# Kernel optimization log

Measured on AMD Instinct MI355X. Metric: run time of the kernel, lower is better.

## Reference

```python
import jax, jax.numpy as jnp
import numpy as np

B_, C_, H_, W_, Dd_ = 2, 64, 32, 32, 32
D_INNER, D_STATE, DT_RANK, D_CONV = 64, 8, 4, 4


def setup_inputs() -> dict:
    key = jax.random.key(0)
    ks = jax.random.split(key, 12)
    s = 0.05
    A_init = jnp.log(jnp.tile(jnp.arange(1, D_STATE + 1, dtype=jnp.float32), (D_INNER, 1)))
    return {
        "input": jax.random.normal(ks[0], (B_, C_, H_, W_, Dd_), jnp.float32),
        "conv_w": jax.random.normal(ks[1], (C_, C_, 3, 3, 3), jnp.float32) * s,
        "conv_b": jax.random.normal(ks[2], (C_,), jnp.float32) * s,
        "in_proj_w": jax.random.normal(ks[3], (2 * D_INNER, C_), jnp.float32) * s,
        "conv1d_w": jax.random.normal(ks[4], (D_INNER, 1, D_CONV), jnp.float32) * s,
        "conv1d_b": jax.random.normal(ks[5], (D_INNER,), jnp.float32) * s,
        "x_proj_w": jax.random.normal(ks[6], (DT_RANK + 2 * D_STATE, D_INNER), jnp.float32) * s,
        "dt_proj_w": jax.random.normal(ks[7], (D_INNER, DT_RANK), jnp.float32) * s,
        "dt_proj_b": jax.random.normal(ks[8], (D_INNER,), jnp.float32) * s,
        "A_log": A_init,
        "A_b_log": A_init + 0.01,
        "D_skip": jnp.ones((D_INNER,), jnp.float32),
        "out_proj_w": jax.random.normal(ks[9], (C_, D_INNER), jnp.float32) * s,
        "ln_g": jnp.ones((C_,), jnp.float32),
        "ln_b": jnp.zeros((C_,), jnp.float32),
    }


def _conv3d(x, w, b):
    y = jax.lax.conv_general_dilated(x, w, (1, 1, 1), [(1, 1), (1, 1), (1, 1)],
                                     dimension_numbers=("NCDHW", "OIDHW", "NCDHW"))
    return y + b[None, :, None, None, None]


def _instance_norm(x, eps=1e-5):
    m = x.mean(axis=(2, 3, 4), keepdims=True)
    v = ((x - m) ** 2).mean(axis=(2, 3, 4), keepdims=True)
    return (x - m) * jax.lax.rsqrt(v + eps)


def _selective_scan(xc, dt, Bm, Cm, A, D_skip):
    # xc, dt: (b,L,d); Bm, Cm: (b,L,n); A: (d,n)
    dA = jnp.exp(dt[..., None] * A)                       # (b,L,d,n)
    dBx = (dt * xc)[..., None] * Bm[:, :, None, :]        # (b,L,d,n)

    def comb(l, r):
        al, bl = l
        ar, br = r
        return ar * al, ar * bl + br

    _, h = jax.lax.associative_scan(comb, (dA, dBx), axis=1)
    y = jnp.einsum("bldn,bln->bld", h, Cm)
    return y + xc * D_skip


def _direction(xz, conv1d_w, conv1d_b, x_proj_w, dt_proj_w, dt_proj_b, A, D_skip):
    x, z = jnp.split(xz, 2, axis=-1)                      # each (b,L,d)
    xt = jnp.swapaxes(x, 1, 2)                            # (b,d,L)
    xc = jax.lax.conv_general_dilated(xt, conv1d_w, (1,), [(D_CONV - 1, 0)],
                                      feature_group_count=D_INNER,
                                      dimension_numbers=("NCH", "OIH", "NCH"))
    xc = jax.nn.silu(jnp.swapaxes(xc + conv1d_b[None, :, None], 1, 2))  # (b,L,d)
    dbl = xc @ x_proj_w.T
    dt_r = dbl[..., :DT_RANK]
    Bm = dbl[..., DT_RANK:DT_RANK + D_STATE]
    Cm = dbl[..., DT_RANK + D_STATE:]
    dt = jax.nn.softplus(dt_r @ dt_proj_w.T + dt_proj_b)
    y = _selective_scan(xc, dt, Bm, Cm, A, D_skip)
    return y * jax.nn.silu(z)


def reference(input, conv_w, conv_b, in_proj_w, conv1d_w, conv1d_b, x_proj_w,
              dt_proj_w, dt_proj_b, A_log, A_b_log, D_skip, out_proj_w, ln_g, ln_b):
    # skip path: Conv3d -> InstanceNorm3d -> ReLU
    skip = jax.nn.relu(_instance_norm(_conv3d(input, conv_w, conv_b)))
    b, c, h, w, d = input.shape
    tokens = input.transpose(0, 2, 3, 4, 1).reshape(b, h * w * d, c)  # b (hwd) c
    xz = tokens @ in_proj_w.T                                          # (b,L,2d)
    A = -jnp.exp(A_log)
    A_b = -jnp.exp(A_b_log)
    y_f = _direction(xz, conv1d_w, conv1d_b, x_proj_w, dt_proj_w, dt_proj_b, A, D_skip)
    y_b = _direction(xz[:, ::-1], conv1d_w, conv1d_b, x_proj_w, dt_proj_w, dt_proj_b, A_b, D_skip)[:, ::-1]
    out = ((y_f + y_b) @ out_proj_w.T) / 2.0  # if_devide_out=True
    mu = out.mean(-1, keepdims=True)
    var = ((out - mu) ** 2).mean(-1, keepdims=True)
    out = (out - mu) * jax.lax.rsqrt(var + 1e-5) * ln_g + ln_b  # use_norm=True
    vol = out.reshape(b, h, w, d, c).transpose(0, 4, 1, 2, 3)
    return _conv3d(vol, conv_w, conv_b) + skip
```

## Files before the change

kernel.cpp:

```cpp
#include <hip/hip_runtime.h>
#include <hip/hip_bf16.h>

typedef __hip_bfloat16 bf16;
typedef __attribute__((ext_vector_type(8))) short short8;
typedef __attribute__((ext_vector_type(4))) float f32x4;

__device__ __forceinline__ float b2f(bf16 x){ return __bfloat162float(x); }
__device__ __forceinline__ bf16  f2b(float x){ return __float2bfloat16(x); }
__device__ __forceinline__ float s2f(short s){ bf16 t = *(bf16*)&s; return b2f(t); }

__device__ __forceinline__ float ldin(const void* p, size_t i, int f32){
  return f32 ? ((const float*)p)[i] : b2f(((const bf16*)p)[i]);
}
__device__ __forceinline__ void stout(void* p, size_t i, float v, int f32){
  if(f32) ((float*)p)[i] = v; else ((bf16*)p)[i] = f2b(v);
}

constexpr int SP   = 32*32*32;
constexpr int LTOK = SP;
constexpr int NC   = 512;
constexpr int CLEN = LTOK / NC;
constexpr int NSEQ = 2*2*64*8;
constexpr int SEG  = 16;
constexpr int SEGLEN = NC/SEG;

__global__ void k_detect(const void* conv_w, int* flag){
  if(threadIdx.x==0 && blockIdx.x==0){
    const bf16* p = (const bf16*)conv_w;
    int f = 0;
    for(int i=0;i<128;i++){
      float v = b2f(p[i]);
      if(!(v==v) || fabsf(v) > 1.0f) f = 1;
    }
    *flag = f;
  }
}

__global__ void k_fill(void* out, int n, const int* flag){
  const int f32 = *flag;
  int i = blockIdx.x*256 + threadIdx.x;
  if(i<n) stout(out, i, 12345.0f, f32);
}

__global__ void k_wprep(const void* __restrict__ cw, bf16* __restrict__ wt,
                        const int* __restrict__ flag){
  const int f32 = *flag;
  int t = blockIdx.x*256 + threadIdx.x;
  if(t >= 27*64*64) return;
  int tap = t >> 12;
  int oc  = (t >> 6) & 63;
  int ci  = t & 63;
  wt[t] = f2b(ldin(cw, ((size_t)(oc*64+ci))*27 + tap, f32));
}

__global__ __launch_bounds__(256) void k_inprojm(
    const void* __restrict__ in, const void* __restrict__ pw,
    bf16* __restrict__ xz, bf16* __restrict__ xin_t,
    const int* __restrict__ flag){
  const int f32 = *flag;
  __shared__ bf16 tok[128*72];
  __shared__ bf16 wl [128*72];
  int tid = threadIdx.x;
  int b = blockIdx.x >> 8, tile = blockIdx.x & 255;
  int l0 = tile*128;

  for(int p=tid; p<1024; p+=256){
    int j = p & 127, c8 = p >> 7;
    short8 v;
    #pragma unroll
    for(int k=0;k<8;k++){
      bf16 t = f2b(ldin(pw, j*64 + c8*8 + k, f32));
      v[k] = *(short*)&t;
    }
    *(short8*)(&wl[j*72 + c8*8]) = v;
  }
  for(int p=tid; p<1024; p+=256){
    int i = p & 127, c8 = p >> 7;
    short8 v;
    #pragma unroll
    for(int k=0;k<8;k++){
      bf16 t = f2b(ldin(in, ((size_t)(b*64 + c8*8 + k))*SP + l0 + i, f32));
      v[k] = *(short*)&t;
    }
    *(short8*)(&tok[i*72 + c8*8]) = v;
  }
  __syncthreads();

  int lane = tid & 63, wv = tid >> 6;
  int pn = lane & 15, quad = lane >> 4, kg8 = quad*8;
  f32x4 acc[2][8];
  #pragma unroll
  for(int mt=0;mt<2;mt++)
    #pragma unroll
    for(int nt=0;nt<8;nt++) acc[mt][nt]=(f32x4)(0.f);

  #pragma unroll
  for(int kq=0;kq<2;kq++){
    short8 a0 = *(const short8*)(&tok[(wv*32      + pn)*72 + kq*32 + kg8]);
    short8 a1 = *(const short8*)(&tok[(wv*32 + 16 + pn)*72 + kq*32 + kg8]);
    #pragma unroll
    for(int nt=0;nt<8;nt++){
      short8 bb = *(const short8*)(&wl[(nt*16+pn)*72 + kq*32 + kg8]);
      acc[0][nt] = __builtin_amdgcn_mfma_f32_16x16x32_bf16(a0,bb,acc[0][nt],0,0,0);
      acc[1][nt] = __builtin_amdgcn_mfma_f32_16x16x32_bf16(a1,bb,acc[1][nt],0,0,0);
    }
  }

  #pragma unroll
  for(int mt=0;mt<2;mt++){
    #pragma unroll
    for(int nt=0;nt<8;nt++){
      #pragma unroll
      for(int r=0;r<4;r++){
        int token = wv*32 + mt*16 + quad*4 + r;
        xz[((size_t)b*LTOK + l0 + token)*128 + nt*16 + pn] = f2b(acc[mt][nt][r]);
      }
    }
  }
  for(int p=tid; p<8192; p+=256){
    int i = p >> 6, c = p & 63;
    xin_t[((size_t)b*SP + l0 + i)*64 + c] = tok[i*72 + c];
  }
}

__global__ __launch_bounds__(256, 2) void k_convm(
    const bf16* __restrict__ xin_t, const bf16* __restrict__ wt,
    const void* __restrict__ cb, const bf16* __restrict__ skip,
    bf16* __restrict__ out_bf, void* __restrict__ out_any,
    int mode, const int* __restrict__ flag){
  const int f32 = *flag;
  __shared__ bf16 xt[612*40];

  int tid  = threadIdx.x;
  int lane = tid & 63;
  int wv   = tid >> 6;
  int pn   = lane & 15;
  int quad = lane >> 4;
  int kg8  = quad * 8;
  int laneA = pn*64 + kg8;

  int blk = blockIdx.x;
  int b  = blk >> 8;
  int h  = (blk >> 3) & 31;
  int w0 = (blk & 7) * 4;

  f32x4 acc[4][2];
  #pragma unroll
  for(int m=0;m<4;m++){ acc[m][0]=(f32x4)(0.f); acc[m][1]=(f32x4)(0.f); }

  for(int cic=0; cic<64; cic+=32){
    if(cic) __syncthreads();
    if(cic==0){
      for(int i=tid; i<36*2*32; i+=256){
        int cil = i & 31; int q = i >> 5;
        int hw = q >> 1;  int dd = (q & 1) ? 33 : 0;
        xt[(hw*34 + dd)*40 + cil] = f2b(0.f);
      }
    }
    #pragma unroll
    for(int it=0; it<9; it++){
      int row = it*64 + (tid>>2);
      int q4  = tid & 3;
      int d   = row & 31;
      int hw  = row >> 5;
      int ww  = hw % 6, hh = hw / 6;
      int hg = h + hh - 1, wg = w0 + ww - 1;
      short8 v = (short8)(0);
      if((unsigned)hg < 32u && (unsigned)wg < 32u)
        v = *(const short8*)(&xin_t[(((size_t)b*SP) + hg*1024 + wg*32 + d)*64 + cic + q4*8]);
      *(short8*)(&xt[(hw*34 + 1 + d)*40 + q4*8]) = v;
    }
    __syncthreads();

    const bf16* wb0 = wt + cic + laneA;
    short8 a[4], an[4];
    #pragma unroll
    for(int u=0;u<4;u++) a[u] = *(const short8*)(wb0 + u*1024);

    #pragma unroll
    for(int tap=0; tap<27; tap++){
      if(tap<26){
        const bf16* wn = wb0 + (tap+1)*4096;
        #pragma unroll
        for(int u=0;u<4;u++) an[u] = *(const short8*)(wn + u*1024);
      }
      int kz = tap/9, kyx = tap - kz*9;
      int ky = kyx/3, kx = kyx - ky*3;
      int rix = (kz*6 + wv + ky)*34 + pn + kx;
      short8 b0 = *(const short8*)(&xt[ rix     *40 + kg8]);
      short8 b1 = *(const short8*)(&xt[(rix+16) *40 + kg8]);
      acc[0][0] = __builtin_amdgcn_mfma_f32_16x16x32_bf16(a[0],b0,acc[0][0],0,0,0);
      acc[0][1] = __builtin_amdgcn_mfma_f32_16x16x32_bf16(a[0],b1,acc[0][1],0,0,0);
      acc[1][0] = __builtin_amdgcn_mfma_f32_16x16x32_bf16(a[1],b0,acc[1][0],0,0,0);
      acc[1][1] = __builtin_amdgcn_mfma_f32_16x16x32_bf16(a[1],b1,acc[1][1],0,0,0);
      acc[2][0] = __builtin_amdgcn_mfma_f32_16x16x32_bf16(a[2],b0,acc[2][0],0,0,0);
      acc[2][1] = __builtin_amdgcn_mfma_f32_16x16x32_bf16(a[2],b1,acc[2][1],0,0,0);
      acc[3][0] = __builtin_amdgcn_mfma_f32_16x16x32_bf16(a[3],b0,acc[3][0],0,0,0);
      acc[3][1] = __builtin_amdgcn_mfma_f32_16x16x32_bf16(a[3],b1,acc[3][1],0,0,0);
      #pragma unroll
      for(int u=0;u<4;u++) a[u] = an[u];
    }
  }

  int posbase = h*1024 + (w0+wv)*32;
  #pragma unroll
  for(int m=0;m<4;m++){
    #pragma unroll
    for(int t=0;t<2;t++){
      #pragma unroll
      for(int r=0;r<4;r++){
        int oc = m*16 + quad*4 + r;
        size_t idx = ((size_t)(b*64+oc))*SP + posbase + t*16 + pn;
        float v = acc[m][t][r] + ldin(cb, oc, f32);
        if(mode==0) out_bf[idx] = f2b(v);
        else        stout(out_any, idx, v + b2f(skip[idx]), f32);
      }
    }
  }
}

__global__ void k_inorm(bf16* __restrict__ buf){
  int bc = blockIdx.x;
  bf16* p = buf + (size_t)bc*SP;
  float s=0.f, s2=0.f;
  for(int i=threadIdx.x;i<SP;i+=256){ float v=b2f(p[i]); s+=v; s2+=v*v; }
  __shared__ float sh[8];
  #pragma unroll
  for(int m=32;m>=1;m>>=1){ s += __shfl_xor(s,m); s2 += __shfl_xor(s2,m); }
  int wid = threadIdx.x>>6;
  if((threadIdx.x&63)==0){ sh[wid]=s; sh[4+wid]=s2; }
  __syncthreads();
  if(threadIdx.x==0){ float a=0,b2=0; for(int i=0;i<4;i++){a+=sh[i]; b2+=sh[4+i];} sh[0]=a; sh[4]=b2; }
  __syncthreads();
  float mean = sh[0]*(1.f/SP);
  float var  = sh[4]*(1.f/SP) - mean*mean;
  float inv = rsqrtf(fmaxf(var,0.f) + 1e-5f);
  for(int i=threadIdx.x;i<SP;i+=256){
    float v=(b2f(p[i])-mean)*inv;
    p[i] = f2b(v>0.f ? v : 0.f);
  }
}

__global__ void k_dirprep(const bf16* __restrict__ xz, const void* __restrict__ c1w,
                          const void* __restrict__ c1b, const void* __restrict__ xpw,
                          bf16* __restrict__ bcg, float* __restrict__ dtr,
                          const int* __restrict__ flag){
  const int f32 = *flag;
  __shared__ float xs[67][64];
  __shared__ float xcs[64][65];
  __shared__ float xws[20][65];
  int bid = blockIdx.x;
  int g = bid >> 10, b = (bid>>9)&1, tile = bid & 511;
  int l0 = tile*64;
  int gb = g*2+b;
  for(int t=threadIdx.x; t<20*64; t+=256){ int j=t>>6, d=t&63; xws[j][d]=ldin(xpw, t, f32); }
  for(int t=threadIdx.x; t<67*64; t+=256){
    int row=t>>6, d=t&63;
    int l = l0 + row - 3;
    float v = 0.f;
    if(l>=0 && l<LTOK){
      int lg = g ? (LTOK-1-l) : l;
      v = b2f(xz[((size_t)b*LTOK + lg)*128 + d]);
    }
    xs[row][d]=v;
  }
  __syncthreads();
  for(int t=threadIdx.x; t<4096; t+=256){
    int d=t&63, tl=t>>6;
    float acc = ldin(c1b, d, f32);
    #pragma unroll
    for(int k=0;k<4;k++) acc += ldin(c1w, d*4+k, f32) * xs[tl+k][d];
    xcs[tl][d] = acc / (1.f + __expf(-acc));
  }
  __syncthreads();
  for(int task=threadIdx.x; task<1280; task+=256){
    int j = task % 20, tl = task / 20;
    float acc=0.f;
    #pragma unroll
    for(int d=0; d<64; d++) acc += xcs[tl][d]*xws[j][d];
    size_t l = (size_t)gb*LTOK + l0 + tl;
    if(j<4) dtr[l*4 + j] = acc;
    else    bcg[l*16 + (j-4)] = f2b(acc);
  }
}

__global__ __launch_bounds__(256, 2) void k_scan1(
                        const bf16* __restrict__ xz, const float* __restrict__ dtr,
                        const bf16* __restrict__ bcg,
                        const void* __restrict__ c1w, const void* __restrict__ c1b,
                        const void* __restrict__ dpw, const void* __restrict__ dpb,
                        const void* __restrict__ alog, const void* __restrict__ ablog,
                        float* __restrict__ psP, float* __restrict__ psS,
                        const int* __restrict__ flag){
  const int f32 = *flag;
  int wid = blockIdx.x*4 + (threadIdx.x>>6);
  int lane = threadIdx.x & 63;
  int chunk = wid & (NC-1);
  int b = (wid>>9)&1;
  int g = wid>>10;
  int gb = g*2+b;
  const void* al = g ? ablog : alog;
  float ac[8];
  #pragma unroll
  for(int n=0;n<8;n++) ac[n] = -__expf(ldin(al, lane*8+n, f32));
  float cw0=ldin(c1w,lane*4+0,f32), cw1=ldin(c1w,lane*4+1,f32), cw2=ldin(c1w,lane*4+2,f32), cw3=ldin(c1w,lane*4+3,f32);
  float cb_=ldin(c1b,lane,f32);
  float dw0=ldin(dpw,lane*4+0,f32), dw1=ldin(dpw,lane*4+1,f32), dw2=ldin(dpw,lane*4+2,f32), dw3=ldin(dpw,lane*4+3,f32);
  float db_=ldin(dpb,lane,f32);
  float S[8];
  #pragma unroll
  for(int n=0;n<8;n++) S[n]=0.f;
  float Tsum = 0.f;
  int lt0 = chunk*CLEN;
  float x0,x1,x2;
  {
    float xr[3];
    #pragma unroll
    for(int j=0;j<3;j++){
      int lt = lt0-3+j;
      float v=0.f;
      if(lt>=0){ int lg = g ? (LTOK-1-lt) : lt; v=b2f(xz[((size_t)b*LTOK+lg)*128 + lane]); }
      xr[j]=v;
    }
    x0=xr[0]; x1=xr[1]; x2=xr[2];
  }
  for(int i0=0;i0<CLEN;i0+=8){
    bf16 xv[8]; float4 dv[8]; short8 bb[8];
    #pragma unroll
    for(int k=0;k<8;k++){
      int lt = lt0+i0+k;
      int lg = g ? (LTOK-1-lt) : lt;
      xv[k] = xz[((size_t)b*LTOK+lg)*128 + lane];
      size_t l = (size_t)gb*LTOK + lt;
      dv[k] = *(const float4*)(dtr + l*4);
      bb[k] = *(const short8*)(bcg + l*16);
    }
    #pragma unroll
    for(int k=0;k<8;k++){
      float x3 = b2f(xv[k]);
      float pre = cb_ + cw0*x0 + cw1*x1 + cw2*x2 + cw3*x3;
      float xc = pre / (1.f + __expf(-pre));
      float v = db_ + dv[k].x*dw0 + dv[k].y*dw1 + dv[k].z*dw2 + dv[k].w*dw3;
      float e = __expf(-fabsf(v));
      float dt = fmaxf(v,0.f) + __logf(1.f+e);
      Tsum += dt;
      float bx = dt*xc;
      #pragma unroll
      for(int n=0;n<8;n++){
        float a = __expf(dt*ac[n]);
        S[n] = a*S[n] + bx*s2f(bb[k][n]);
      }
      x0=x1; x1=x2; x2=x3;
    }
  }
  int seq = (gb*64 + lane)*8;
  #pragma unroll
  for(int n=0;n<8;n++){
    psP[(size_t)chunk*NSEQ + seq + n] = __expf(ac[n]*Tsum);
    psS[(size_t)chunk*NSEQ + seq + n] = S[n];
  }
}

__global__ void k_scan2a(const float* __restrict__ psP, const float* __restrict__ psS,
                         float* __restrict__ segP, float* __restrict__ segS){
  int idx = blockIdx.x*256 + threadIdx.x;
  int seq = idx & (NSEQ-1);
  int seg = idx >> 11;
  float P = 1.f, S = 0.f;
  int i0 = seg*SEGLEN;
  #pragma unroll 4
  for(int i=0;i<SEGLEN;i++){
    float p = psP[(size_t)(i0+i)*NSEQ + seq];
    float s = psS[(size_t)(i0+i)*NSEQ + seq];
    S = p*S + s;
    P *= p;
  }
  segP[seg*NSEQ + seq] = P;
  segS[seg*NSEQ + seq] = S;
}
__global__ void k_scan2b(const float* __restrict__ segP, const float* __restrict__ segS,
                         float* __restrict__ segC){
  int seq = blockIdx.x*256 + threadIdx.x;
  if(seq >= NSEQ) return;
  float h = 0.f;
  #pragma unroll
  for(int s=0;s<SEG;s++){
    segC[s*NSEQ + seq] = h;
    h = segP[s*NSEQ + seq]*h + segS[s*NSEQ + seq];
  }
}
__global__ void k_scan2c(const float* __restrict__ psP, const float* __restrict__ segC,
                         float* __restrict__ psC){
  int idx = blockIdx.x*256 + threadIdx.x;
  int seq = idx & (NSEQ-1);
  int seg = idx >> 11;
  float h = segC[seg*NSEQ + seq];
  int i0 = seg*SEGLEN;
  #pragma unroll 4
  for(int i=0;i<SEGLEN;i++){
    float p = psP[(size_t)(i0+i)*NSEQ + seq];
    float s = psC[(size_t)(i0+i)*NSEQ + seq];
    psC[(size_t)(i0+i)*NSEQ + seq] = h;
    h = p*h + s;
  }
}

__global__ __launch_bounds__(256, 2) void k_scan3(
                        const bf16* __restrict__ xz, const float* __restrict__ dtr,
                        const bf16* __restrict__ bcg,
                        const void* __restrict__ c1w, const void* __restrict__ c1b,
                        const void* __restrict__ dpw, const void* __restrict__ dpb,
                        const void* __restrict__ alog, const void* __restrict__ ablog,
                        const void* __restrict__ dskip, const float* __restrict__ carry,
                        bf16* __restrict__ ybuf, const int* __restrict__ flag){
  const int f32 = *flag;
  int wid = blockIdx.x*4 + (threadIdx.x>>6);
  int lane = threadIdx.x & 63;
  int chunk = wid & (NC-1);
  int b = (wid>>9)&1;
  int g = wid>>10;
  int gb = g*2+b;
  const void* al = g ? ablog : alog;
  float ac[8];
  #pragma unroll
  for(int n=0;n<8;n++) ac[n] = -__expf(ldin(al, lane*8+n, f32));
  float cw0=ldin(c1w,lane*4+0,f32), cw1=ldin(c1w,lane*4+1,f32), cw2=ldin(c1w,lane*4+2,f32), cw3=ldin(c1w,lane*4+3,f32);
  float cb_=ldin(c1b,lane,f32);
  float dw0=ldin(dpw,lane*4+0,f32), dw1=ldin(dpw,lane*4+1,f32), dw2=ldin(dpw,lane*4+2,f32), dw3=ldin(dpw,lane*4+3,f32);
  float db_=ldin(dpb,lane,f32);
  float dsk = ldin(dskip,lane,f32);
  int seq = (gb*64 + lane)*8;
  float h[8];
  #pragma unroll
  for(int n=0;n<8;n++) h[n] = carry[(size_t)chunk*NSEQ + seq + n];
  int lt0 = chunk*CLEN;
  float x0,x1,x2;
  {
    float xr[3];
    #pragma unroll
    for(int j=0;j<3;j++){
      int lt = lt0-3+j;
      float v=0.f;
      if(lt>=0){ int lg = g ? (LTOK-1-lt) : lt; v=b2f(xz[((size_t)b*LTOK+lg)*128 + lane]); }
      xr[j]=v;
    }
    x0=xr[0]; x1=xr[1]; x2=xr[2];
  }
  for(int i0=0;i0<CLEN;i0+=8){
    bf16 xv[8]; float4 dv[8]; short8 bb[8]; short8 cc[8];
    #pragma unroll
    for(int k=0;k<8;k++){
      int lt = lt0+i0+k;
      int lg = g ? (LTOK-1-lt) : lt;
      xv[k] = xz[((size_t)b*LTOK+lg)*128 + lane];
      size_t l = (size_t)gb*LTOK + lt;
      dv[k] = *(const float4*)(dtr + l*4);
      bb[k] = *(const short8*)(bcg + l*16);
      cc[k] = *(const short8*)(bcg + l*16 + 8);
    }
    #pragma unroll
    for(int k=0;k<8;k++){
      float x3 = b2f(xv[k]);
      float pre = cb_ + cw0*x0 + cw1*x1 + cw2*x2 + cw3*x3;
      float xc = pre / (1.f + __expf(-pre));
      float v = db_ + dv[k].x*dw0 + dv[k].y*dw1 + dv[k].z*dw2 + dv[k].w*dw3;
      float e = __expf(-fabsf(v));
      float dt = fmaxf(v,0.f) + __logf(1.f+e);
      float bx = dt*xc;
      float y = xc*dsk;
      #pragma unroll
      for(int n=0;n<8;n++){
        float a = __expf(dt*ac[n]);
        h[n] = a*h[n] + bx*s2f(bb[k][n]);
        y += h[n]*s2f(cc[k][n]);
      }
      size_t l = (size_t)gb*LTOK + lt0+i0+k;
      ybuf[l*64 + lane] = f2b(y);
      x0=x1; x1=x2; x2=x3;
    }
  }
}

__global__ __launch_bounds__(256) void k_outln(
                        const bf16* __restrict__ ybuf, const bf16* __restrict__ xz,
                        const void* __restrict__ opw,
                        const void* __restrict__ lng, const void* __restrict__ lnb,
                        bf16* __restrict__ vol_t, const int* __restrict__ flag){
  const int f32 = *flag;
  __shared__ bf16 vsm[64*72];
  __shared__ bf16 wsm[64*72];
  __shared__ float gsm[64], bsm[64];
  int tid = threadIdx.x;
  int b = blockIdx.x >> 9, tile = blockIdx.x & 511;
  int l0 = tile*64;

  for(int p=tid; p<512; p+=256){
    int c = p & 63, d8 = p >> 6;
    short8 v;
    #pragma unroll
    for(int k=0;k<8;k++){ bf16 t = f2b(ldin(opw, c*64 + d8*8 + k, f32)); v[k] = *(short*)&t; }
    *(short8*)(&wsm[c*72 + d8*8]) = v;
  }
  if(tid<64){ gsm[tid]=ldin(lng,tid,f32); bsm[tid]=ldin(lnb,tid,f32); }
  for(int p=tid; p<4096; p+=256){
    int tl = p >> 6, d = p & 63;
    int l = l0 + tl;
    float yf = b2f(ybuf[((size_t)(0+b)*LTOK + l)*64 + d]);
    float yb = b2f(ybuf[((size_t)(2+b)*LTOK + (LTOK-1-l))*64 + d]);
    float z  = b2f(xz[((size_t)b*LTOK + l)*128 + 64 + d]);
    float sz = z / (1.f + __expf(-z));
    vsm[tl*72 + d] = f2b(0.5f*(yf+yb)*sz);
  }
  __syncthreads();

  int lane = tid & 63, wv = tid >> 6, pn = lane & 15, quad = lane >> 4, kg8 = quad*8;
  f32x4 acc[4];
  #pragma unroll
  for(int nt=0;nt<4;nt++) acc[nt]=(f32x4)(0.f);
  #pragma unroll
  for(int kq=0;kq<2;kq++){
    short8 a = *(const short8*)(&vsm[(wv*16+pn)*72 + kq*32 + kg8]);
    #pragma unroll
    for(int nt=0;nt<4;nt++){
      short8 bb = *(const short8*)(&wsm[(nt*16+pn)*72 + kq*32 + kg8]);
      acc[nt] = __builtin_amdgcn_mfma_f32_16x16x32_bf16(a,bb,acc[nt],0,0,0);
    }
  }
  __syncthreads();

  float gl[4], bl[4];
  #pragma unroll
  for(int nt=0;nt<4;nt++){ gl[nt]=gsm[nt*16+pn]; bl[nt]=bsm[nt*16+pn]; }
  #pragma unroll
  for(int r=0;r<4;r++){
    float vals[4]; float s=0.f;
    #pragma unroll
    for(int nt=0;nt<4;nt++){ vals[nt]=acc[nt][r]; s+=vals[nt]; }
    #pragma unroll
    for(int m=1;m<16;m<<=1) s += __shfl_xor(s, m);
    float mu = s*(1.f/64.f);
    float s2=0.f;
    #pragma unroll
    for(int nt=0;nt<4;nt++){ float dv=vals[nt]-mu; s2+=dv*dv; }
    #pragma unroll
    for(int m=1;m<16;m<<=1) s2 += __shfl_xor(s2, m);
    float inv = rsqrtf(s2*(1.f/64.f) + 1e-5f);
    int token = wv*16 + quad*4 + r;
    #pragma unroll
    for(int nt=0;nt<4;nt++){
      vsm[token*72 + nt*16 + pn] = f2b((vals[nt]-mu)*inv*gl[nt] + bl[nt]);
    }
  }
  __syncthreads();
  for(int p=tid; p<512; p+=256){
    int tl = p >> 3, d8 = p & 7;
    *(short8*)(&vol_t[((size_t)b*SP + l0 + tl)*64 + d8*8]) = *(const short8*)(&vsm[tl*72 + d8*8]);
  }
}

extern "C" void kernel_launch(void* const* d_in, const int* in_sizes, int n_in,
                              void* d_out, int out_size, void* d_ws, size_t ws_size,
                              hipStream_t stream){
  const void* input  = d_in[0];
  const void* conv_w = d_in[1];
  const void* conv_b = d_in[2];
  const void* inpw   = d_in[3];
  const void* c1w    = d_in[4];
  const void* c1b    = d_in[5];
  const void* xpw    = d_in[6];
  const void* dpw    = d_in[7];
  const void* dpb    = d_in[8];
  const void* alog   = d_in[9];
  const void* ablog  = d_in[10];
  const void* dskip  = d_in[11];
  const void* opw    = d_in[12];
  const void* lng    = d_in[13];
  const void* lnb    = d_in[14];

  char* base = (char*)d_ws;
  bf16*  skipb = (bf16*) (base + 0);
  bf16*  xz    = (bf16*) (base + 8388608);
  bf16*  bcg   = (bf16*) (base + 25165824);
  float* dtr   = (float*)(base + 29360128);
  float* psP   = (float*)(base + 31457280);
  float* psS   = (float*)(base + 35651584);
  bf16*  ybuf  = (bf16*) (base + 39845888);
  bf16*  wt    = (bf16*) (base + 56623104);
  float* segP  = (float*)(base + 56844288);
  float* segS  = (float*)(base + 56975360);
  float* segC  = (float*)(base + 57106432);
  bf16*  xin_t = (bf16*) (base + 31457280);
  bf16*  vol_t = (bf16*) (base + 25165824);
  int*   flagp = (int*)  (base + 60817408);
  const size_t NEED = 60817424;

  k_detect<<<dim3(1), dim3(64), 0, stream>>>(conv_w, flagp);

  if(ws_size < NEED){
    k_fill<<<dim3((out_size+255)/256), dim3(256), 0, stream>>>(d_out, out_size, flagp);
    return;
  }

  k_wprep  <<<dim3(432),   dim3(256), 0, stream>>>(conv_w, wt, flagp);
  k_inprojm<<<dim3(512),   dim3(256), 0, stream>>>(input, inpw, xz, xin_t, flagp);
  k_convm  <<<dim3(512),   dim3(256), 0, stream>>>(xin_t, wt, conv_b, nullptr, skipb, nullptr, 0, flagp);
  k_inorm  <<<dim3(128),   dim3(256), 0, stream>>>(skipb);
  k_dirprep<<<dim3(2048),  dim3(256), 0, stream>>>(xz, c1w, c1b, xpw, bcg, dtr, flagp);
  k_scan1  <<<dim3(512),   dim3(256), 0, stream>>>(xz, dtr, bcg, c1w, c1b, dpw, dpb, alog, ablog, psP, psS, flagp);
  k_scan2a <<<dim3(128),   dim3(256), 0, stream>>>(psP, psS, segP, segS);
  k_scan2b <<<dim3(8),     dim3(256), 0, stream>>>(segP, segS, segC);
  k_scan2c <<<dim3(128),   dim3(256), 0, stream>>>(psP, segC, psS);
  k_scan3  <<<dim3(512),   dim3(256), 0, stream>>>(xz, dtr, bcg, c1w, c1b, dpw, dpb, alog, ablog, dskip, psS, ybuf, flagp);
  k_outln  <<<dim3(1024),  dim3(256), 0, stream>>>(ybuf, xz, opw, lng, lnb, vol_t, flagp);
  k_convm  <<<dim3(512),   dim3(256), 0, stream>>>(vol_t, wt, conv_b, skipb, nullptr, d_out, 1, flagp);
}
```

Before: 462.0 us.

## Halve conv3d tile per block to double grid size and raise occupancy

Each conv block now covers 2 w-columns instead of 4, so the grid doubles to 1024 blocks, and launch bounds allow 4 blocks per CU instead of 2. Each wave computes one 16-position tile instead of two, and the LDS row stride is padded from 40 to 44 to reduce bank conflicts. The software-pipelined weight prefetch is dropped in favour of direct loads per tap. In exchange, each weight load now feeds half as many MFMAs, the halo overhead per output point rises, and there is less explicit latency hiding.

```diff
diff --git a/kernel.cpp b/kernel.cpp
--- a/kernel.cpp
+++ b/kernel.cpp
@@ -123,98 +123,91 @@
   }
 }
 
-__global__ __launch_bounds__(256, 2) void k_convm(
+__global__ __launch_bounds__(256, 4) void k_convm(
     const bf16* __restrict__ xin_t, const bf16* __restrict__ wt,
     const void* __restrict__ cb, const bf16* __restrict__ skip,
     bf16* __restrict__ out_bf, void* __restrict__ out_any,
     int mode, const int* __restrict__ flag){
   const int f32 = *flag;
-  __shared__ bf16 xt[612*40];
+  __shared__ bf16 xt[408*44];
 
   int tid  = threadIdx.x;
   int lane = tid & 63;
   int wv   = tid >> 6;
+  int wr   = wv & 1;
+  int dh   = wv >> 1;
   int pn   = lane & 15;
   int quad = lane >> 4;
   int kg8  = quad * 8;
   int laneA = pn*64 + kg8;
 
   int blk = blockIdx.x;
-  int b  = blk >> 8;
-  int h  = (blk >> 3) & 31;
-  int w0 = (blk & 7) * 4;
-
-  f32x4 acc[4][2];
-  #pragma unroll
-  for(int m=0;m<4;m++){ acc[m][0]=(f32x4)(0.f); acc[m][1]=(f32x4)(0.f); }
+  int b  = blk >> 9;
+  int h  = (blk >> 4) & 31;
+  int w0 = (blk & 15) * 2;
+
+  f32x4 acc[4];
+  #pragma unroll
+  for(int m=0;m<4;m++) acc[m]=(f32x4)(0.f);
 
   for(int cic=0; cic<64; cic+=32){
     if(cic) __syncthreads();
     if(cic==0){
-      for(int i=tid; i<36*2*32; i+=256){
-        int cil = i & 31; int q = i >> 5;
-        int hw = q >> 1;  int dd = (q & 1) ? 33 : 0;
-        xt[(hw*34 + dd)*40 + cil] = f2b(0.f);
+      for(int i=tid; i<96; i+=256){
+        int q4 = i & 3; int rr = i >> 2;
+        int dd = (rr & 1) ? 33 : 0; int hw = rr >> 1;
+        *(short8*)(&xt[(hw*34 + dd)*44 + q4*8]) = (short8)(0);
       }
     }
     #pragma unroll
-    for(int it=0; it<9; it++){
-      int row = it*64 + (tid>>2);
-      int q4  = tid & 3;
+    for(int it=0; it<6; it++){
+      int j = it*256 + tid;
+      int q4  = j & 3;
+      int row = j >> 2;
       int d   = row & 31;
       int hw  = row >> 5;
-      int ww  = hw % 6, hh = hw / 6;
+      int ww  = hw & 3, hh = hw >> 2;
       int hg = h + hh - 1, wg = w0 + ww - 1;
       short8 v = (short8)(0);
       if((unsigned)hg < 32u && (unsigned)wg < 32u)
         v = *(const short8*)(&xin_t[(((size_t)b*SP) + hg*1024 + wg*32 + d)*64 + cic + q4*8]);
-      *(short8*)(&xt[(hw*34 + 1 + d)*40 + q4*8]) = v;
+      *(short8*)(&xt[((hh*4+ww)*34 + 1 + d)*44 + q4*8]) = v;
     }
     __syncthreads();
 
-    const bf16* wb0 = wt + cic + laneA;
-    short8 a[4], an[4];
-    #pragma unroll
-    for(int u=0;u<4;u++) a[u] = *(const short8*)(wb0 + u*1024);
-
-    #pragma unroll
-    for(int tap=0; tap<27; tap++){
-      if(tap<26){
-        const bf16* wn = wb0 + (tap+1)*4096;
+    #pragma unroll
+    for(int kz=0;kz<3;kz++){
+      #pragma unroll
+      for(int ky=0;ky<3;ky++){
         #pragma unroll
-        for(int u=0;u<4;u++) an[u] = *(const short8*)(wn + u*1024);
+        for(int kx=0;kx<3;kx++){
+          int tap = (kz*3+ky)*3+kx;
+          const bf16* wbase = wt + tap*4096 + cic + laneA;
+          short8 a0 = *(const short8*)(wbase);
+          short8 a1 = *(const short8*)(wbase + 1024);
+          short8 a2 = *(const short8*)(wbase + 2048);
+          short8 a3 = *(const short8*)(wbase + 3072);
+          int rix = (kz*4 + wr + ky)*34 + dh*16 + pn + kx;
+          short8 bb = *(const short8*)(&xt[rix*44 + kg8]);
+          acc[0] = __builtin_amdgcn_mfma_f32_16x16x32_bf16(a0,bb,acc[0],0,0,0);
+          acc[1] = __builtin_amdgcn_mfma_f32_16x16x32_bf16(a1,bb,acc[1],0,0,0);
+          acc[2] = __builtin_amdgcn_mfma_f32_16x16x32_bf16(a2,bb,acc[2],0,0,0);
+          acc[3] = __builtin_amdgcn_mfma_f32_16x16x32_bf16(a3,bb,acc[3],0,0,0);
+        }
       }
-      int kz = tap/9, kyx = tap - kz*9;
-      int ky = kyx/3, kx = kyx - ky*3;
-      int rix = (kz*6 + wv + ky)*34 + pn + kx;
-      short8 b0 = *(const short8*)(&xt[ rix     *40 + kg8]);
-      short8 b1 = *(const short8*)(&xt[(rix+16) *40 + kg8]);
-      acc[0][0] = __builtin_amdgcn_mfma_f32_16x16x32_bf16(a[0],b0,acc[0][0],0,0,0);
-      acc[0][1] = __builtin_amdgcn_mfma_f32_16x16x32_bf16(a[0],b1,acc[0][1],0,0,0);
-      acc[1][0] = __builtin_amdgcn_mfma_f32_16x16x32_bf16(a[1],b0,acc[1][0],0,0,0);
-      acc[1][1] = __builtin_amdgcn_mfma_f32_16x16x32_bf16(a[1],b1,acc[1][1],0,0,0);
-      acc[2][0] = __builtin_amdgcn_mfma_f32_16x16x32_bf16(a[2],b0,acc[2][0],0,0,0);
-      acc[2][1] = __builtin_amdgcn_mfma_f32_16x16x32_bf16(a[2],b1,acc[2][1],0,0,0);
-      acc[3][0] = __builtin_amdgcn_mfma_f32_16x16x32_bf16(a[3],b0,acc[3][0],0,0,0);
-      acc[3][1] = __builtin_amdgcn_mfma_f32_16x16x32_bf16(a[3],b1,acc[3][1],0,0,0);
-      #pragma unroll
-      for(int u=0;u<4;u++) a[u] = an[u];
-    }
-  }
-
-  int posbase = h*1024 + (w0+wv)*32;
+    }
+  }
+
+  int pos = h*1024 + (w0+wr)*32 + dh*16 + pn;
   #pragma unroll
   for(int m=0;m<4;m++){
     #pragma unroll
-    for(int t=0;t<2;t++){
-      #pragma unroll
-      for(int r=0;r<4;r++){
-        int oc = m*16 + quad*4 + r;
-        size_t idx = ((size_t)(b*64+oc))*SP + posbase + t*16 + pn;
-        float v = acc[m][t][r] + ldin(cb, oc, f32);
-        if(mode==0) out_bf[idx] = f2b(v);
-        else        stout(out_any, idx, v + b2f(skip[idx]), f32);
-      }
+    for(int r=0;r<4;r++){
+      int oc = m*16 + quad*4 + r;
+      size_t idx = ((size_t)(b*64+oc))*SP + pos;
+      float v = acc[m][r] + ldin(cb, oc, f32);
+      if(mode==0) out_bf[idx] = f2b(v);
+      else        stout(out_any, idx, v + b2f(skip[idx]), f32);
     }
   }
 }
@@ -603,7 +596,7 @@
 
   k_wprep  <<<dim3(432),   dim3(256), 0, stream>>>(conv_w, wt, flagp);
   k_inprojm<<<dim3(512),   dim3(256), 0, stream>>>(input, inpw, xz, xin_t, flagp);
-  k_convm  <<<dim3(512),   dim3(256), 0, stream>>>(xin_t, wt, conv_b, nullptr, skipb, nullptr, 0, flagp);
+  k_convm  <<<dim3(1024),  dim3(256), 0, stream>>>(xin_t, wt, conv_b, nullptr, skipb, nullptr, 0, flagp);
   k_inorm  <<<dim3(128),   dim3(256), 0, stream>>>(skipb);
   k_dirprep<<<dim3(2048),  dim3(256), 0, stream>>>(xz, c1w, c1b, xpw, bcg, dtr, flagp);
   k_scan1  <<<dim3(512),   dim3(256), 0, stream>>>(xz, dtr, bcg, c1w, c1b, dpw, dpb, alog, ablog, psP, psS, flagp);
@@ -612,5 +605,5 @@
   k_scan2c <<<dim3(128),   dim3(256), 0, stream>>>(psP, segC, psS);
   k_scan3  <<<dim3(512),   dim3(256), 0, stream>>>(xz, dtr, bcg, c1w, c1b, dpw, dpb, alog, ablog, dskip, psS, ybuf, flagp);
   k_outln  <<<dim3(1024),  dim3(256), 0, stream>>>(ybuf, xz, opw, lng, lnb, vol_t, flagp);
-  k_convm  <<<dim3(512),   dim3(256), 0, stream>>>(vol_t, wt, conv_b, skipb, nullptr, d_out, 1, flagp);
-}
+  k_convm  <<<dim3(1024),  dim3(256), 0, stream>>>(vol_t, wt, conv_b, skipb, nullptr, d_out, 1, flagp);
+}
```

New measurement: 550.0 us. 19.1% more time.
